# Performance work log

Measured on AMD Instinct MI355X. Metric: run time of the kernel, lower is better.

## Reference

```python
import jax, jax.numpy as jnp
import numpy as np

N_NODES = 100000
N_EDGES = 1600000
IN_DIM = 128
HID_DIM = 128
OUT_DIM = 64


def gcn_conv(x, W, b, edge_index):
    """GCNConv with add_self_loops, symmetric degree norm, add-aggregation.

    Math matches PyG: out[i] = sum_{(j,i) in E+selfloops} norm_ji * (x_j @ W) + b
    Since lin is linear and there is no edge_attr, we transform x once before
    the gather instead of per-edge (identical result, far less FLOPs/traffic).
    """
    n = x.shape[0]
    loop = jnp.arange(n, dtype=edge_index.dtype)
    row = jnp.concatenate([edge_index[0], loop])  # source nodes (x_j)
    col = jnp.concatenate([edge_index[1], loop])  # destination nodes
    # degree over destinations (includes self loops -> deg >= 1, no div by 0)
    deg = jax.ops.segment_sum(jnp.ones_like(col, dtype=x.dtype), col, num_segments=n)
    dinv = jax.lax.rsqrt(deg)
    norm = dinv[row] * dinv[col]  # [E+N]
    h = x @ W  # [N, out] transform once
    msg = norm[:, None] * h[row]  # [E+N, out] gathered per-edge messages
    out = jax.ops.segment_sum(msg, col, num_segments=n)  # scatter-add
    return out + b


def setup_inputs() -> dict:
    key = jax.random.key(0)
    k1, k2, k3, k4 = jax.random.split(key, 4)
    x = jax.random.normal(k1, (N_NODES, IN_DIM), dtype=jnp.float32)
    edge_index = jax.random.randint(k2, (2, N_EDGES), 0, N_NODES, dtype=jnp.int64)
    # glorot-ish init
    W1 = jax.random.normal(k3, (IN_DIM, HID_DIM), dtype=jnp.float32) * (2.0 / (IN_DIM + HID_DIM)) ** 0.5
    W2 = jax.random.normal(k4, (HID_DIM, OUT_DIM), dtype=jnp.float32) * (2.0 / (HID_DIM + OUT_DIM)) ** 0.5
    b1 = jnp.zeros((HID_DIM,), dtype=jnp.float32)
    b2 = jnp.zeros((OUT_DIM,), dtype=jnp.float32)
    return {"x": x, "edge_index": edge_index, "W1": W1, "b1": b1, "W2": W2, "b2": b2}


def reference(x, edge_index, W1, b1, W2, b2):
    # GCN.forward with prompt_type=None, pooling=False, eval mode (dropout is identity)
    h = gcn_conv(x, W1, b1, edge_index)
    h = jax.nn.relu(h)
    out = gcn_conv(h, W2, b2, edge_index)
    return out
```

## Files before the change

kernel.cpp:

```cpp
#include <hip/hip_runtime.h>


#define DIN 128
#define DHID 128
#define DOUT 64
#define ELLW 64
#define GPART 8
#define BPG 256

typedef __attribute__((ext_vector_type(4))) float f32x4;
typedef __attribute__((ext_vector_type(8))) short bf16x8;
typedef __attribute__((ext_vector_type(4))) int i32x4;

__device__ __forceinline__ float bf2f(unsigned int u16) {
    return __uint_as_float(u16 << 16);
}
__device__ __forceinline__ unsigned short f2bf(float f) {
    unsigned int u = __float_as_uint(f);
    u += 0x7fffu + ((u >> 16) & 1u);
    return (unsigned short)(u >> 16);
}
__device__ __forceinline__ unsigned int pack2(float a, float b) {
    return (unsigned int)f2bf(a) | ((unsigned int)f2bf(b) << 16);
}

__global__ __launch_bounds__(256) void k_packW(const float* __restrict__ W1,
                                               const float* __restrict__ W2,
                                               unsigned short* __restrict__ w1p,
                                               unsigned short* __restrict__ w2p) {
    int id = blockIdx.x * 256 + threadIdx.x;
    if (id < 2048) {
        int lane = id & 63, s = (id >> 6) & 3, t = id >> 8;
        int n = t * 16 + (lane & 15);
        int k0 = s * 32 + (lane >> 4) * 8;
#pragma unroll
        for (int j = 0; j < 8; ++j)
            w1p[(size_t)id * 8 + j] = f2bf(W1[(k0 + j) * DHID + n]);
    } else if (id < 3072) {
        int id2 = id - 2048;
        int lane = id2 & 63, s = (id2 >> 6) & 3, t = id2 >> 8;
        int n = t * 16 + (lane & 15);
        int k0 = s * 32 + (lane >> 4) * 8;
#pragma unroll
        for (int j = 0; j < 8; ++j)
            w2p[(size_t)id2 * 8 + j] = f2bf(W2[(k0 + j) * DOUT + n]);
    }
}

__device__ __forceinline__ void fill_edge(int c, int r, int lo, int hi,
                                          int* __restrict__ deg, int* __restrict__ ell) {
    if (c >= lo && c < hi) {
        int k = atomicAdd(&deg[c], 1);
        if (k < ELLW) ell[(size_t)c * ELLW + k] = r;
    }
}

__global__ __launch_bounds__(256) void k_fill_gemm1(
        const int* __restrict__ rows, const int* __restrict__ cols,
        int* __restrict__ deg, int* __restrict__ ell,
        int E, int perBlock, int R, int FB,
        const float* __restrict__ x, const unsigned short* __restrict__ w1p,
        unsigned short* __restrict__ h1b, int N) {
    if ((int)blockIdx.x < FB) {
        int g  = blockIdx.x & (GPART - 1);
        int cb = blockIdx.x >> 3;
        int lo = g * R, hi = lo + R;
        int eBeg = cb * perBlock;
        int eEnd = eBeg + perBlock; if (eEnd > E) eEnd = E;
        for (int e = eBeg + 4 * threadIdx.x; e < eEnd; e += 4 * 256) {
            if (e + 3 < eEnd) {
                i32x4 c4 = __builtin_nontemporal_load((const i32x4*)(cols + e));
                i32x4 r4 = __builtin_nontemporal_load((const i32x4*)(rows + e));
                fill_edge(c4.x, r4.x, lo, hi, deg, ell);
                fill_edge(c4.y, r4.y, lo, hi, deg, ell);
                fill_edge(c4.z, r4.z, lo, hi, deg, ell);
                fill_edge(c4.w, r4.w, lo, hi, deg, ell);
            } else {
                for (int j = e; j < eEnd; ++j) fill_edge(cols[j], rows[j], lo, hi, deg, ell);
            }
        }
        return;
    }
    int bid = blockIdx.x - FB;
    int wave = threadIdx.x >> 6, lane = threadIdx.x & 63;
    int quad = lane >> 4, qr = lane & 15;
    int rowBase = bid * 64 + wave * 16;
    int arow = rowBase + qr;
    bool rowOK = arow < N;
    f32x4 acc[8] = {};
#pragma unroll
    for (int s = 0; s < 4; ++s) {
        bf16x8 a = {};
        if (rowOK) {
            const float* ap = x + (size_t)arow * DIN + s * 32 + quad * 8;
            float4 lo = *(const float4*)ap;
            float4 hi = *(const float4*)(ap + 4);
            a[0] = (short)f2bf(lo.x); a[1] = (short)f2bf(lo.y);
            a[2] = (short)f2bf(lo.z); a[3] = (short)f2bf(lo.w);
            a[4] = (short)f2bf(hi.x); a[5] = (short)f2bf(hi.y);
            a[6] = (short)f2bf(hi.z); a[7] = (short)f2bf(hi.w);
        }
#pragma unroll
        for (int t = 0; t < 8; ++t) {
            bf16x8 b = *(const bf16x8*)(w1p + ((size_t)(t * 4 + s) * 64 + lane) * 8);
            acc[t] = __builtin_amdgcn_mfma_f32_16x16x32_bf16(a, b, acc[t], 0, 0, 0);
        }
    }
#pragma unroll
    for (int t = 0; t < 8; ++t)
#pragma unroll
        for (int i = 0; i < 4; ++i) {
            int r = rowBase + quad * 4 + i;
            if (r < N) h1b[(size_t)r * DHID + t * 16 + qr] = f2bf(acc[t][i]);
        }
}

__global__ __launch_bounds__(256) void k_gather1(const int* __restrict__ deg,
                                                 const int* __restrict__ ell,
                                                 const unsigned int* __restrict__ h1u,
                                                 const float* __restrict__ b1,
                                                 unsigned int* __restrict__ hactu, int N) {
    int w = (blockIdx.x * 256 + threadIdx.x) >> 6;
    int lane = threadIdx.x & 63;
    if (w >= N) return;
    int dfull = deg[w];
    int d = dfull > ELLW ? ELLW : dfull;
    int iv = ell[(size_t)w * ELLW + lane];
    float dv = (lane < d) ? rsqrtf((float)(deg[iv] + 1)) : 0.f;
    float a0 = 0.f, a1 = 0.f;
    int e = 0;
    for (; e + 8 <= d; e += 8) {
        int s[8]; float wg[8]; unsigned int v[8];
#pragma unroll
        for (int j = 0; j < 8; ++j) { s[j] = __shfl(iv, e + j); wg[j] = __shfl(dv, e + j); }
#pragma unroll
        for (int j = 0; j < 8; ++j) v[j] = h1u[(size_t)s[j] * 64 + lane];
#pragma unroll
        for (int j = 0; j < 8; ++j) {
            a0 = fmaf(wg[j], bf2f(v[j] & 0xffffu), a0);
            a1 = fmaf(wg[j], bf2f(v[j] >> 16), a1);
        }
    }
    for (; e + 4 <= d; e += 4) {
        int s[4]; float wg[4]; unsigned int v[4];
#pragma unroll
        for (int j = 0; j < 4; ++j) { s[j] = __shfl(iv, e + j); wg[j] = __shfl(dv, e + j); }
#pragma unroll
        for (int j = 0; j < 4; ++j) v[j] = h1u[(size_t)s[j] * 64 + lane];
#pragma unroll
        for (int j = 0; j < 4; ++j) {
            a0 = fmaf(wg[j], bf2f(v[j] & 0xffffu), a0);
            a1 = fmaf(wg[j], bf2f(v[j] >> 16), a1);
        }
    }
    for (; e < d; ++e) {
        int s0 = __shfl(iv, e);
        float w0 = __shfl(dv, e);
        unsigned int v0 = h1u[(size_t)s0 * 64 + lane];
        a0 = fmaf(w0, bf2f(v0 & 0xffffu), a0); a1 = fmaf(w0, bf2f(v0 >> 16), a1);
    }
    float di = rsqrtf((float)(dfull + 1)), self = di * di;
    unsigned int hv = h1u[(size_t)w * 64 + lane];
    float2 bv = *(const float2*)(b1 + 2 * lane);
    float r0 = fmaf(di, a0, fmaf(self, bf2f(hv & 0xffffu), bv.x));
    float r1 = fmaf(di, a1, fmaf(self, bf2f(hv >> 16), bv.y));
    hactu[(size_t)w * 64 + lane] = pack2(fmaxf(r0, 0.f), fmaxf(r1, 0.f));
}

__global__ __launch_bounds__(256) void k_gemm2(const unsigned short* __restrict__ hactb,
                                               const unsigned short* __restrict__ w2p,
                                               unsigned short* __restrict__ h2b, int N) {
    int wave = threadIdx.x >> 6, lane = threadIdx.x & 63;
    int quad = lane >> 4, qr = lane & 15;
    int rowBase = blockIdx.x * 64 + wave * 16;
    int arow = rowBase + qr;
    bool rowOK = arow < N;
    f32x4 acc[4] = {};
#pragma unroll
    for (int s = 0; s < 4; ++s) {
        bf16x8 a = {};
        if (rowOK) a = *(const bf16x8*)(hactb + (size_t)arow * DHID + s * 32 + quad * 8);
#pragma unroll
        for (int t = 0; t < 4; ++t) {
            bf16x8 b = *(const bf16x8*)(w2p + ((size_t)(t * 4 + s) * 64 + lane) * 8);
            acc[t] = __builtin_amdgcn_mfma_f32_16x16x32_bf16(a, b, acc[t], 0, 0, 0);
        }
    }
#pragma unroll
    for (int t = 0; t < 4; ++t)
#pragma unroll
        for (int i = 0; i < 4; ++i) {
            int r = rowBase + quad * 4 + i;
            if (r < N) h2b[(size_t)r * DOUT + t * 16 + qr] = f2bf(acc[t][i]);
        }
}

__global__ __launch_bounds__(256) void k_gather2(const int* __restrict__ deg,
                                                 const int* __restrict__ ell,
                                                 const unsigned short* __restrict__ h2u,
                                                 const float* __restrict__ b2,
                                                 float* __restrict__ out, int N) {
    int w = (blockIdx.x * 256 + threadIdx.x) >> 6;
    int lane = threadIdx.x & 63;
    if (w >= N) return;
    int dfull = deg[w];
    int d = dfull > ELLW ? ELLW : dfull;
    int iv = ell[(size_t)w * ELLW + lane];
    float dv = (lane < d) ? rsqrtf((float)(deg[iv] + 1)) : 0.f;
    float a = 0.f;
    int e = 0;
    for (; e + 8 <= d; e += 8) {
        int s[8]; float wg[8]; float v[8];
#pragma unroll
        for (int j = 0; j < 8; ++j) { s[j] = __shfl(iv, e + j); wg[j] = __shfl(dv, e + j); }
#pragma unroll
        for (int j = 0; j < 8; ++j) v[j] = bf2f((unsigned int)h2u[(size_t)s[j] * DOUT + lane]);
#pragma unroll
        for (int j = 0; j < 8; ++j) a = fmaf(wg[j], v[j], a);
    }
    for (; e + 4 <= d; e += 4) {
        int s[4]; float wg[4]; float v[4];
#pragma unroll
        for (int j = 0; j < 4; ++j) { s[j] = __shfl(iv, e + j); wg[j] = __shfl(dv, e + j); }
#pragma unroll
        for (int j = 0; j < 4; ++j) v[j] = bf2f((unsigned int)h2u[(size_t)s[j] * DOUT + lane]);
#pragma unroll
        for (int j = 0; j < 4; ++j) a = fmaf(wg[j], v[j], a);
    }
    for (; e < d; ++e) {
        int s0 = __shfl(iv, e);
        float w0 = __shfl(dv, e);
        a = fmaf(w0, bf2f((unsigned int)h2u[(size_t)s0 * DOUT + lane]), a);
    }
    float di = rsqrtf((float)(dfull + 1)), self = di * di;
    float hv = bf2f((unsigned int)h2u[(size_t)w * DOUT + lane]);
    out[(size_t)w * DOUT + lane] = fmaf(di, a, fmaf(self, hv, b2[lane]));
}

extern "C" void kernel_launch(void* const* d_in, const int* in_sizes, int n_in,
                              void* d_out, int out_size, void* d_ws, size_t ws_size,
                              hipStream_t stream) {
    const float* x  = (const float*)d_in[0];
    const int*   ei = (const int*)d_in[1];
    const float* W1 = (const float*)d_in[2];
    const float* b1 = (const float*)d_in[3];
    const float* W2 = (const float*)d_in[4];
    const float* b2 = (const float*)d_in[5];

    const int N = in_sizes[0] / DIN;
    const int E = in_sizes[1] / 2;
    const int* rows = ei;
    const int* cols = ei + E;

    char* p = (char*)d_ws;
    int*   ell  = (int*)p;                    p += (size_t)N * ELLW * 4;
    unsigned short* h1b = (unsigned short*)p;   p += (size_t)N * DHID * 2;
    unsigned short* hactb = (unsigned short*)p; p += (size_t)N * DHID * 2;
    unsigned short* w1p = (unsigned short*)p;   p += (size_t)2048 * 8 * 2;
    unsigned short* w2p = (unsigned short*)p;   p += (size_t)1024 * 8 * 2;
    int*   deg  = (int*)p;                    p += (size_t)N * 4;
    unsigned short* h2b = h1b;

    const int R = (N + GPART - 1) / GPART;
    int perBlock = (E + BPG - 1) / BPG;
    perBlock = (perBlock + 3) & ~3;
    const int FB = GPART * BPG;
    const int GB = (N + 63) / 64;

    k_packW<<<12, 256, 0, stream>>>(W1, W2, w1p, w2p);
    (void)hipMemsetAsync(deg, 0, (size_t)N * 4, stream);

    k_fill_gemm1<<<FB + GB, 256, 0, stream>>>(rows, cols, deg, ell, E, perBlock, R, FB,
                                              x, w1p, h1b, N);

    k_gather1<<<(N + 3) / 4, 256, 0, stream>>>(deg, ell, (const unsigned int*)h1b,
                                               b1, (unsigned int*)hactb, N);

    k_gemm2<<<(N + 63) / 64, 256, 0, stream>>>(hactb, w2p, h2b, N);
    k_gather2<<<(N + 3) / 4, 256, 0, stream>>>(deg, ell, h2b, b2, (float*)d_out, N);
}
```

Baseline: 313.6 us.

## Bind edge-fill partitions to XCD id with per-partition dynamic chunk queues

Fill blocks now take their destination-node partition from the hardware XCC_ID register rather than from the block index. Each block then pulls 2048-edge chunks from a per-partition atomic counter until none are left. The goal is to keep the degree and ELL atomics for a partition within one XCD's L2 and to balance fill work dynamically across blocks. The cost is an extra atomic plus two barriers per chunk. Correctness also depends on every XCD getting at least one fill block, because otherwise a partition would never be filled.

```diff
diff --git a/kernel.cpp b/kernel.cpp
--- a/kernel.cpp
+++ b/kernel.cpp
@@ -6,7 +6,7 @@
 #define DOUT 64
 #define ELLW 64
 #define GPART 8
-#define BPG 256
+#define CHUNKE 2048
 
 typedef __attribute__((ext_vector_type(4))) float f32x4;
 typedef __attribute__((ext_vector_type(8))) short bf16x8;
@@ -57,26 +57,34 @@
 
 __global__ __launch_bounds__(256) void k_fill_gemm1(
         const int* __restrict__ rows, const int* __restrict__ cols,
-        int* __restrict__ deg, int* __restrict__ ell,
-        int E, int perBlock, int R, int FB,
+        int* __restrict__ deg, int* __restrict__ ell, int* __restrict__ qcur,
+        int E, int R, int FB, int NCHUNK,
         const float* __restrict__ x, const unsigned short* __restrict__ w1p,
         unsigned short* __restrict__ h1b, int N) {
     if ((int)blockIdx.x < FB) {
-        int g  = blockIdx.x & (GPART - 1);
-        int cb = blockIdx.x >> 3;
-        int lo = g * R, hi = lo + R;
-        int eBeg = cb * perBlock;
-        int eEnd = eBeg + perBlock; if (eEnd > E) eEnd = E;
-        for (int e = eBeg + 4 * threadIdx.x; e < eEnd; e += 4 * 256) {
-            if (e + 3 < eEnd) {
-                i32x4 c4 = __builtin_nontemporal_load((const i32x4*)(cols + e));
-                i32x4 r4 = __builtin_nontemporal_load((const i32x4*)(rows + e));
-                fill_edge(c4.x, r4.x, lo, hi, deg, ell);
-                fill_edge(c4.y, r4.y, lo, hi, deg, ell);
-                fill_edge(c4.z, r4.z, lo, hi, deg, ell);
-                fill_edge(c4.w, r4.w, lo, hi, deg, ell);
-            } else {
-                for (int j = e; j < eEnd; ++j) fill_edge(cols[j], rows[j], lo, hi, deg, ell);
+        __shared__ int sChunk;
+        unsigned g = __builtin_amdgcn_s_getreg((7 << 11) | 20) & (GPART - 1);
+        int lo = g * R;
+        int hi = lo + R; if (hi > N) hi = N;
+        for (;;) {
+            if (threadIdx.x == 0) sChunk = atomicAdd(&qcur[g], 1);
+            __syncthreads();
+            int chunk = sChunk;
+            __syncthreads();
+            if (chunk >= NCHUNK) break;
+            int eBeg = chunk * CHUNKE;
+            int eEnd = eBeg + CHUNKE; if (eEnd > E) eEnd = E;
+            for (int e = eBeg + 4 * threadIdx.x; e < eEnd; e += 4 * 256) {
+                if (e + 3 < eEnd) {
+                    i32x4 c4 = __builtin_nontemporal_load((const i32x4*)(cols + e));
+                    i32x4 r4 = __builtin_nontemporal_load((const i32x4*)(rows + e));
+                    fill_edge(c4.x, r4.x, lo, hi, deg, ell);
+                    fill_edge(c4.y, r4.y, lo, hi, deg, ell);
+                    fill_edge(c4.z, r4.z, lo, hi, deg, ell);
+                    fill_edge(c4.w, r4.w, lo, hi, deg, ell);
+                } else {
+                    for (int j = e; j < eEnd; ++j) fill_edge(cols[j], rows[j], lo, hi, deg, ell);
+                }
             }
         }
         return;
@@ -259,19 +267,19 @@
     unsigned short* w1p = (unsigned short*)p;   p += (size_t)2048 * 8 * 2;
     unsigned short* w2p = (unsigned short*)p;   p += (size_t)1024 * 8 * 2;
     int*   deg  = (int*)p;                    p += (size_t)N * 4;
+    int*   qcur = (int*)p;                    p += (size_t)GPART * 4;
     unsigned short* h2b = h1b;
 
     const int R = (N + GPART - 1) / GPART;
-    int perBlock = (E + BPG - 1) / BPG;
-    perBlock = (perBlock + 3) & ~3;
-    const int FB = GPART * BPG;
+    const int NCHUNK = (E + CHUNKE - 1) / CHUNKE;
+    const int FB = 2048;
     const int GB = (N + 63) / 64;
 
     k_packW<<<12, 256, 0, stream>>>(W1, W2, w1p, w2p);
-    (void)hipMemsetAsync(deg, 0, (size_t)N * 4, stream);
-
-    k_fill_gemm1<<<FB + GB, 256, 0, stream>>>(rows, cols, deg, ell, E, perBlock, R, FB,
-                                              x, w1p, h1b, N);
+    (void)hipMemsetAsync(deg, 0, (size_t)N * 4 + (size_t)GPART * 4, stream);
+
+    k_fill_gemm1<<<FB + GB, 256, 0, stream>>>(rows, cols, deg, ell, qcur,
+                                              E, R, FB, NCHUNK, x, w1p, h1b, N);
 
     k_gather1<<<(N + 3) / 4, 256, 0, stream>>>(deg, ell, (const unsigned int*)h1b,
                                                b1, (unsigned int*)hactb, N);
```

Result: slower. 366.2 us (+16.8%).
